# Optimization experiments

Hardware: AMD Instinct MI355X
Metric: run time of the kernel (lower is better)

The kernel has to match this reference:

```python
import jax, jax.numpy as jnp
import numpy as np

DIM = 1024
H = 16          # num query heads
KV = 8          # num kv heads
HD = DIM // H   # head_dim = 64
B, P = 8, 1024


def setup_inputs() -> dict:
    key = jax.random.key(0)
    ks = jax.random.split(key, 6)
    s = 0.02
    return {
        "x": jax.random.normal(ks[0], (B, P, DIM), dtype=jnp.float32),
        "Wq": jax.random.normal(ks[1], (DIM, DIM), dtype=jnp.float32) * s,
        "Wk": jax.random.normal(ks[2], (KV * HD, DIM), dtype=jnp.float32) * s,
        "Wv": jax.random.normal(ks[3], (KV * HD, DIM), dtype=jnp.float32) * s,
        "Wp": jax.random.normal(ks[4], (DIM, DIM), dtype=jnp.float32) * s,
        "bp": jax.random.normal(ks[5], (DIM,), dtype=jnp.float32) * s,
    }


def _q_allocations(k):
    # k: (B, KV, P, HD). k_norms: frobenius norm over (P, HD), summed over batch.
    kn = jnp.sqrt(jnp.sum(k * k, axis=(2, 3))).sum(axis=0)  # (KV,)
    kn = (kn - kn.min()) / (kn.max() - kn.min())
    alloc = jnp.round(kn / kn.sum() * H).astype(jnp.int32)   # (KV,)
    # fix up so alloc.sum() == H (mirrors the torch while-loops)
    alloc = jax.lax.while_loop(lambda a: a.sum() > H,
                               lambda a: a.at[jnp.argmax(a)].add(-1), alloc)
    alloc = jax.lax.while_loop(lambda a: a.sum() < H,
                               lambda a: a.at[jnp.argmin(a)].add(1), alloc)
    return alloc


def reference(x, Wq, Wk, Wv, Wp, bp):
    Bx, Px, C = x.shape
    scale = HD ** -0.5
    q = (x @ Wq.T).reshape(Bx, Px, H, HD).transpose(0, 2, 1, 3) * scale  # (B,H,P,HD)
    k = (x @ Wk.T).reshape(Bx, Px, KV, HD).transpose(0, 2, 1, 3)         # (B,KV,P,HD)
    v = (x @ Wv.T).reshape(Bx, Px, KV, HD).transpose(0, 2, 1, 3)

    alloc = _q_allocations(k)  # (KV,) sums to H
    # query head h belongs to kv group i where cumsum[i-1] <= h < cumsum[i].
    # Equivalent to torch.split(q, alloc) + per-group attention, because the
    # per-group softmax over keys is independent per query head.
    kv_idx = jnp.searchsorted(jnp.cumsum(alloc), jnp.arange(H), side='right')
    k_g = jnp.take(k, kv_idx, axis=1)  # (B,H,P,HD)
    v_g = jnp.take(v, kv_idx, axis=1)

    scores = jnp.einsum('bhqd,bhkd->bhqk', q, k_g)
    weights = jax.nn.softmax(scores, axis=-1)
    out = jnp.einsum('bhqk,bhkd->bhqd', weights, v_g)  # (B,H,P,HD)
    out = out.transpose(0, 2, 1, 3).reshape(Bx, Px, C)
    return out @ Wp.T + bp
```

## Files before the change

### kernel.cpp

```cpp
#include <hip/hip_runtime.h>
#include <stdint.h>


typedef float f32x4 __attribute__((ext_vector_type(4)));
typedef short s16x8 __attribute__((ext_vector_type(8)));
typedef short s16x4 __attribute__((ext_vector_type(4)));
typedef int   i32x4 __attribute__((ext_vector_type(4)));

__device__ __forceinline__ unsigned short f2bf(float f) {
  unsigned int u = __builtin_bit_cast(unsigned int, f);
  u = (u + 0x7FFFu + ((u >> 16) & 1u)) >> 16;
  return (unsigned short)u;
}
__device__ __forceinline__ float bf2f(unsigned short h) {
  unsigned int u = ((unsigned int)h) << 16;
  return __builtin_bit_cast(float, u);
}

__device__ __forceinline__ unsigned int pk_bf16(float a, float b) {
#if __has_builtin(__builtin_amdgcn_cvt_pk_bf16_f32)
  auto v = __builtin_amdgcn_cvt_pk_bf16_f32(a, b);
  return __builtin_bit_cast(unsigned int, v);
#else
  unsigned int ua = __builtin_bit_cast(unsigned int, a);
  unsigned int ub = __builtin_bit_cast(unsigned int, b);
  ua += 0x7FFFu + ((ua >> 16) & 1u);
  ub += 0x7FFFu + ((ub >> 16) & 1u);
#if __has_builtin(__builtin_amdgcn_perm)
  return __builtin_amdgcn_perm(ub, ua, 0x07060302);
#else
  return (ua >> 16) | (ub & 0xFFFF0000u);
#endif
#endif
}

__device__ __forceinline__ unsigned int perm_half(unsigned int hi, unsigned int lo, int takeHi) {
#if __has_builtin(__builtin_amdgcn_perm)
  return __builtin_amdgcn_perm(hi, lo, takeHi ? 0x07060302u : 0x05040100u);
#else
  return takeHi ? ((lo >> 16) | (hi & 0xFFFF0000u)) : ((lo & 0xFFFFu) | (hi << 16));
#endif
}

__device__ __forceinline__ float fast_exp2(float x) {
#if __has_builtin(__builtin_amdgcn_exp2f)
  return __builtin_amdgcn_exp2f(x);
#else
  return exp2f(x);
#endif
}

#if __has_builtin(__builtin_amdgcn_global_load_lds)
#define HAVE_GLL 1
typedef const __attribute__((address_space(1))) void* gas_ptr;
typedef __attribute__((address_space(3))) void* las_ptr;
__device__ __forceinline__ void gll16(const void* g, void* l) {
  __builtin_amdgcn_global_load_lds((gas_ptr)g, (las_ptr)l, 16, 0, 0);
}
#endif

__global__ void convert_kernel(const float* __restrict__ x, const float* __restrict__ Wq,
                               const float* __restrict__ Wk, const float* __restrict__ Wv,
                               const float* __restrict__ Wp,
                               unsigned short* __restrict__ xb,
                               unsigned short* __restrict__ wqkv,
                               unsigned short* __restrict__ wpb,
                               float* __restrict__ sums) {
  if (blockIdx.x == 0 && threadIdx.x < 64) sums[threadIdx.x] = 0.0f;
  const long i = ((long)blockIdx.x * 256 + threadIdx.x) * 4;
  const float* src; unsigned short* dst; long off; float scale = 1.0f;
  if (i < 8388608L)       { src = x;  dst = xb;             off = i;             }
  else if (i < 9437184L)  { src = Wq; dst = wqkv;           off = i - 8388608L;  scale = 0.18033688011112042f; }
  else if (i < 9961472L)  { src = Wk; dst = wqkv + 1048576; off = i - 9437184L;  }
  else if (i < 10485760L) { src = Wv; dst = wqkv + 1572864; off = i - 9961472L;  }
  else                    { src = Wp; dst = wpb;            off = i - 10485760L; }
  f32x4 v = *(const f32x4*)(src + off);
  s16x4 o;
  o[0] = (short)f2bf(v[0] * scale);
  o[1] = (short)f2bf(v[1] * scale);
  o[2] = (short)f2bf(v[2] * scale);
  o[3] = (short)f2bf(v[3] * scale);
  *(s16x4*)(dst + off) = o;
}

template<int N, bool OUT_BF16, bool DO_SUMSQ>
__global__ __launch_bounds__(256)
void gemm_bt(const unsigned short* __restrict__ A,
             const unsigned short* __restrict__ Bw,
             unsigned short* __restrict__ Cb,
             float* __restrict__ Cf,
             const float* __restrict__ bias,
             float* __restrict__ sums) {
  __shared__ __align__(16) unsigned short As[8192];
  __shared__ __align__(16) unsigned short Bs[8192];
  constexpr int NB = N / 128;
  const int bm = blockIdx.x / NB, bn = blockIdx.x % NB;
  const int m0 = bm * 128, n0 = bn * 128;
  const int t = threadIdx.x;
  const int w = t >> 6, lane = t & 63, quad = lane >> 4, ln = lane & 15;
  const int wm = w & 1, wn = w >> 1;

  const int lrow = lane >> 3;
  const int lc8  = ((lane & 7) ^ lrow) << 3;
  const unsigned short* agl = A  + (m0 + w * 32 + lrow) * 1024 + lc8;
  const unsigned short* bgl = Bw + (n0 + w * 32 + lrow) * 1024 + lc8;

  f32x4 acc[4][4] = {};

  for (int k0 = 0; k0 < 1024; k0 += 64) {
    __syncthreads();
#ifdef HAVE_GLL
    #pragma unroll
    for (int c = 0; c < 4; ++c) {
      gll16(agl + k0 + c * 8192, &As[w * 2048 + c * 512]);
      gll16(bgl + k0 + c * 8192, &Bs[w * 2048 + c * 512]);
    }
#else
    i32x4 ra[4], rb[4];
    #pragma unroll
    for (int c = 0; c < 4; ++c) {
      ra[c] = *(const i32x4*)(agl + k0 + c * 8192);
      rb[c] = *(const i32x4*)(bgl + k0 + c * 8192);
    }
    #pragma unroll
    for (int c = 0; c < 4; ++c) {
      *(i32x4*)(&As[w * 2048 + c * 512 + lane * 8]) = ra[c];
      *(i32x4*)(&Bs[w * 2048 + c * 512 + lane * 8]) = rb[c];
    }
#endif
    __syncthreads();
    #pragma unroll
    for (int kc = 0; kc < 2; ++kc) {
      const int pcs = ((kc * 4 + quad) ^ (ln & 7)) << 3;
      s16x8 af[4], bf[4];
      #pragma unroll
      for (int i = 0; i < 4; ++i)
        af[i] = *(const s16x8*)(&As[(wm * 64 + i * 16 + ln) * 64 + pcs]);
      #pragma unroll
      for (int j = 0; j < 4; ++j)
        bf[j] = *(const s16x8*)(&Bs[(wn * 64 + j * 16 + ln) * 64 + pcs]);
      #pragma unroll
      for (int i = 0; i < 4; ++i)
        #pragma unroll
        for (int j = 0; j < 4; ++j)
          acc[i][j] = __builtin_amdgcn_mfma_f32_16x16x32_bf16(af[i], bf[j], acc[i][j], 0, 0, 0);
    }
  }

  if constexpr (DO_SUMSQ) {
    if (bn >= 8 && bn < 12) {
      float ss = 0.0f;
      #pragma unroll
      for (int i = 0; i < 4; ++i)
        #pragma unroll
        for (int j = 0; j < 4; ++j)
          #pragma unroll
          for (int r = 0; r < 4; ++r)
            ss += acc[i][j][r] * acc[i][j][r];
      #pragma unroll
      for (int off = 1; off < 64; off <<= 1) ss += __shfl_xor(ss, off);
      if (lane == 0)
        atomicAdd(&sums[(m0 >> 10) * 8 + (bn - 8) * 2 + wn], ss);
    }
  }

  #pragma unroll
  for (int j = 0; j < 4; ++j) {
    const int gn = n0 + wn * 64 + j * 16 + ln;
    float bv = 0.0f;
    if constexpr (!OUT_BF16) bv = bias[gn];
    #pragma unroll
    for (int i = 0; i < 4; ++i) {
      const int gm0 = m0 + wm * 64 + i * 16 + quad * 4;
      #pragma unroll
      for (int r = 0; r < 4; ++r) {
        float v = acc[i][j][r];
        if constexpr (OUT_BF16) Cb[(gm0 + r) * N + gn] = f2bf(v);
        else                    Cf[(gm0 + r) * N + gn] = v + bv;
      }
    }
  }
}

__global__ __launch_bounds__(256, 4)
void attn_kernel(const unsigned short* __restrict__ qkv,
                 const float* __restrict__ sums,
                 unsigned short* __restrict__ att) {
  __shared__ __align__(16) unsigned short Ks[4096];
  __shared__ __align__(16) unsigned short Vt[64][72];
  __shared__ __align__(16) unsigned int  Plb[4][32][36];
  __shared__ int kvs;

  const int bid = blockIdx.x;
  const int h = bid & 15, qt = (bid >> 4) & 7, b = bid >> 7;
  const int t = threadIdx.x, w = t >> 6, lane = t & 63, quad = lane >> 4, ln = lane & 15;

  if (t == 0) {
    float kn[8];
    for (int kv = 0; kv < 8; ++kv) {
      float s = 0.0f;
      for (int bb = 0; bb < 8; ++bb) s += sqrtf(sums[bb * 8 + kv]);
      kn[kv] = s;
    }
    float mn = kn[0], mx = kn[0];
    for (int i = 1; i < 8; ++i) { mn = fminf(mn, kn[i]); mx = fmaxf(mx, kn[i]); }
    float tot = 0.0f;
    for (int i = 0; i < 8; ++i) { kn[i] = (kn[i] - mn) / (mx - mn); tot += kn[i]; }
    int a[8], sum = 0;
    for (int i = 0; i < 8; ++i) { a[i] = (int)rintf(kn[i] * 16.0f / tot); sum += a[i]; }
    while (sum > 16) {
      int im = 0;
      for (int i = 1; i < 8; ++i) if (a[i] > a[im]) im = i;
      a[im]--; sum--;
    }
    while (sum < 16) {
      int im = 0;
      for (int i = 1; i < 8; ++i) if (a[i] < a[im]) im = i;
      a[im]++; sum++;
    }
    int cum = 0, idx = 0, c[8];
    for (int i = 0; i < 8; ++i) { cum += a[i]; c[i] = cum; }
    while (c[idx] <= h) idx++;
    kvs = idx;
  }
  __syncthreads();
  const int kvi = kvs;

  s16x8 qf[2][2];
  #pragma unroll
  for (int s = 0; s < 2; ++s) {
    const unsigned short* qp = qkv + (b * 1024 + qt * 128 + s * 64 + w * 16 + ln) * 2048
                               + h * 64 + quad * 8;
    qf[s][0] = *(const s16x8*)(qp);
    qf[s][1] = *(const s16x8*)(qp + 32);
  }

  const int lc8 = ((lane & 7) ^ (lane >> 3)) << 3;
  const unsigned short* kglA = qkv + (b * 1024 + w * 16 + (lane >> 3)) * 2048
                               + 1024 + kvi * 64 + lc8;
  const unsigned short* kglB = kglA + 8 * 2048;

  const int kp = t & 31, vd0 = (t >> 5) << 3;
  const unsigned short* vbase = qkv + (b * 1024 + 2 * kp) * 2048 + 1536 + kvi * 64 + vd0;

  s16x8 ones;
  #pragma unroll
  for (int j = 0; j < 8; ++j) ones[j] = (short)0x3F80;

  f32x4 Oa[2][4] = {};
  f32x4 lacc[2] = {};

  s16x8 va0 = *(const s16x8*)(vbase);
  s16x8 va1 = *(const s16x8*)(vbase + 2048);

  for (int kt = 0; kt < 16; ++kt) {
    __syncthreads();
#ifdef HAVE_GLL
    gll16(kglA + kt * 131072, Ks + w * 1024);
    gll16(kglB + kt * 131072, Ks + w * 1024 + 512);
#else
    i32x4 t0 = *(const i32x4*)(kglA + kt * 131072);
    i32x4 t1 = *(const i32x4*)(kglB + kt * 131072);
    *(i32x4*)(Ks + w * 1024 + lane * 8) = t0;
    *(i32x4*)(Ks + w * 1024 + 512 + lane * 8) = t1;
#endif
    #pragma unroll
    for (int i = 0; i < 8; ++i) {
      unsigned int pk = (unsigned int)(unsigned short)va0[i] |
                        ((unsigned int)(unsigned short)va1[i] << 16);
      *(unsigned int*)(&Vt[vd0 + i][2 * kp]) = pk;
    }
    __syncthreads();

    if (kt < 15) {
      const unsigned short* q = vbase + (kt + 1) * 131072;
      va0 = *(const s16x8*)(q);
      va1 = *(const s16x8*)(q + 2048);
    }

    #pragma unroll
    for (int s = 0; s < 2; ++s) {
      f32x4 sacc[4] = {};
      #pragma unroll
      for (int ks = 0; ks < 4; ++ks) {
        const int r0 = (ks * 16 + ln) * 64;
        s16x8 kf0 = *(const s16x8*)(Ks + r0 + (((quad    ) ^ (ln & 7)) << 3));
        s16x8 kf1 = *(const s16x8*)(Ks + r0 + (((quad + 4) ^ (ln & 7)) << 3));
        sacc[ks] = __builtin_amdgcn_mfma_f32_16x16x32_bf16(qf[s][0], kf0, sacc[ks], 0, 0, 0);
        sacc[ks] = __builtin_amdgcn_mfma_f32_16x16x32_bf16(qf[s][1], kf1, sacc[ks], 0, 0, 0);
      }
      #pragma unroll
      for (int r = 0; r < 4; ++r) {
        unsigned int d0 = pk_bf16(fast_exp2(sacc[0][r]), fast_exp2(sacc[1][r]));
        unsigned int d1 = pk_bf16(fast_exp2(sacc[2][r]), fast_exp2(sacc[3][r]));
        unsigned int* pr = &Plb[w][s * 16 + quad * 4 + r][0];
        pr[ln]      = d0;
        pr[ln + 16] = d1;
      }
    }
    __asm__ volatile("s_waitcnt lgkmcnt(0)" ::: "memory");

    #pragma unroll
    for (int kc = 0; kc < 2; ++kc) {
      s16x8 pf[2];
      #pragma unroll
      for (int s = 0; s < 2; ++s) {
        const unsigned int* base = &Plb[w][s * 16 + ln][kc * 16 + (quad & 1) * 8];
        i32x4 u0 = *(const i32x4*)(base);
        i32x4 u1 = *(const i32x4*)(base + 4);
        const int th = quad >> 1;
        i32x4 pp;
        pp[0] = (int)perm_half((unsigned)u0[1], (unsigned)u0[0], th);
        pp[1] = (int)perm_half((unsigned)u0[3], (unsigned)u0[2], th);
        pp[2] = (int)perm_half((unsigned)u1[1], (unsigned)u1[0], th);
        pp[3] = (int)perm_half((unsigned)u1[3], (unsigned)u1[2], th);
        pf[s] = __builtin_bit_cast(s16x8, pp);
      }
      #pragma unroll
      for (int ds = 0; ds < 4; ++ds) {
        s16x8 vf = *(const s16x8*)(&Vt[ds * 16 + ln][kc * 32 + quad * 8]);
        Oa[0][ds] = __builtin_amdgcn_mfma_f32_16x16x32_bf16(pf[0], vf, Oa[0][ds], 0, 0, 0);
        Oa[1][ds] = __builtin_amdgcn_mfma_f32_16x16x32_bf16(pf[1], vf, Oa[1][ds], 0, 0, 0);
      }
      lacc[0] = __builtin_amdgcn_mfma_f32_16x16x32_bf16(pf[0], ones, lacc[0], 0, 0, 0);
      lacc[1] = __builtin_amdgcn_mfma_f32_16x16x32_bf16(pf[1], ones, lacc[1], 0, 0, 0);
    }
  }

  #pragma unroll
  for (int s = 0; s < 2; ++s) {
    float inv[4];
    #pragma unroll
    for (int r = 0; r < 4; ++r) inv[r] = 1.0f / lacc[s][r];
    const int orow = b * 1024 + qt * 128 + s * 64 + w * 16 + quad * 4;
    #pragma unroll
    for (int ds = 0; ds < 4; ++ds)
      #pragma unroll
      for (int r = 0; r < 4; ++r)
        att[(orow + r) * 1024 + h * 64 + ds * 16 + ln] = f2bf(Oa[s][ds][r] * inv[r]);
  }
}

extern "C" void kernel_launch(void* const* d_in, const int* in_sizes, int n_in,
                              void* d_out, int out_size, void* d_ws, size_t ws_size,
                              hipStream_t stream) {
  const float* x  = (const float*)d_in[0];
  const float* Wq = (const float*)d_in[1];
  const float* Wk = (const float*)d_in[2];
  const float* Wv = (const float*)d_in[3];
  const float* Wp = (const float*)d_in[4];
  const float* bp = (const float*)d_in[5];

  char* ws = (char*)d_ws;
  unsigned short* xb   = (unsigned short*)(ws);
  unsigned short* wqkv = (unsigned short*)(ws + 16777216);
  unsigned short* wpb  = (unsigned short*)(ws + 20971520);
  unsigned short* qkv  = (unsigned short*)(ws + 23068672);
  float*          sums = (float*)(ws + 56623104);
  unsigned short* att  = xb;

  convert_kernel<<<11264, 256, 0, stream>>>(x, Wq, Wk, Wv, Wp, xb, wqkv, wpb, sums);
  gemm_bt<2048, true, true><<<1024, 256, 0, stream>>>(xb, wqkv, qkv, nullptr, nullptr, sums);
  attn_kernel<<<1024, 256, 0, stream>>>(qkv, sums, att);
  gemm_bt<1024, false, false><<<512, 256, 0, stream>>>(att, wpb, nullptr, (float*)d_out, bp, nullptr);
}
```

Measured before the change: 219.9 us.

## Load K fragments directly from global into registers, dropping the LDS K tile

The attention kernel stops staging K tiles through shared memory. Each wave now loads its K MFMA fragments straight from global memory into registers, prefetching the next tile while the current one is processed. This removes the LDS writes, swizzled reads and some synchronization traffic for K. In exchange every wave redundantly fetches the full K tile from global/L2 and register pressure rises, so launch bounds drop from 4 to 3 blocks per CU.

```diff
diff --git a/kernel.cpp b/kernel.cpp
--- a/kernel.cpp
+++ b/kernel.cpp
@@ -11,10 +11,6 @@
   unsigned int u = __builtin_bit_cast(unsigned int, f);
   u = (u + 0x7FFFu + ((u >> 16) & 1u)) >> 16;
   return (unsigned short)u;
-}
-__device__ __forceinline__ float bf2f(unsigned short h) {
-  unsigned int u = ((unsigned int)h) << 16;
-  return __builtin_bit_cast(float, u);
 }
 
 __device__ __forceinline__ unsigned int pk_bf16(float a, float b) {
@@ -182,11 +178,10 @@
   }
 }
 
-__global__ __launch_bounds__(256, 4)
+__global__ __launch_bounds__(256, 3)
 void attn_kernel(const unsigned short* __restrict__ qkv,
                  const float* __restrict__ sums,
                  unsigned short* __restrict__ att) {
-  __shared__ __align__(16) unsigned short Ks[4096];
   __shared__ __align__(16) unsigned short Vt[64][72];
   __shared__ __align__(16) unsigned int  Plb[4][32][36];
   __shared__ int kvs;
@@ -235,10 +230,7 @@
     qf[s][1] = *(const s16x8*)(qp + 32);
   }
 
-  const int lc8 = ((lane & 7) ^ (lane >> 3)) << 3;
-  const unsigned short* kglA = qkv + (b * 1024 + w * 16 + (lane >> 3)) * 2048
-                               + 1024 + kvi * 64 + lc8;
-  const unsigned short* kglB = kglA + 8 * 2048;
+  const unsigned short* kg0 = qkv + (b * 1024 + ln) * 2048 + 1024 + kvi * 64 + quad * 8;
 
   const int kp = t & 31, vd0 = (t >> 5) << 3;
   const unsigned short* vbase = qkv + (b * 1024 + 2 * kp) * 2048 + 1536 + kvi * 64 + vd0;
@@ -252,18 +244,15 @@
 
   s16x8 va0 = *(const s16x8*)(vbase);
   s16x8 va1 = *(const s16x8*)(vbase + 2048);
+  s16x8 kf[2][4];
+  #pragma unroll
+  for (int kc = 0; kc < 2; ++kc)
+    #pragma unroll
+    for (int ks = 0; ks < 4; ++ks)
+      kf[kc][ks] = *(const s16x8*)(kg0 + (long)(ks * 16) * 2048 + kc * 32);
 
   for (int kt = 0; kt < 16; ++kt) {
     __syncthreads();
-#ifdef HAVE_GLL
-    gll16(kglA + kt * 131072, Ks + w * 1024);
-    gll16(kglB + kt * 131072, Ks + w * 1024 + 512);
-#else
-    i32x4 t0 = *(const i32x4*)(kglA + kt * 131072);
-    i32x4 t1 = *(const i32x4*)(kglB + kt * 131072);
-    *(i32x4*)(Ks + w * 1024 + lane * 8) = t0;
-    *(i32x4*)(Ks + w * 1024 + 512 + lane * 8) = t1;
-#endif
     #pragma unroll
     for (int i = 0; i < 8; ++i) {
       unsigned int pk = (unsigned int)(unsigned short)va0[i] |
@@ -283,11 +272,8 @@
       f32x4 sacc[4] = {};
       #pragma unroll
       for (int ks = 0; ks < 4; ++ks) {
-        const int r0 = (ks * 16 + ln) * 64;
-        s16x8 kf0 = *(const s16x8*)(Ks + r0 + (((quad    ) ^ (ln & 7)) << 3));
-        s16x8 kf1 = *(const s16x8*)(Ks + r0 + (((quad + 4) ^ (ln & 7)) << 3));
-        sacc[ks] = __builtin_amdgcn_mfma_f32_16x16x32_bf16(qf[s][0], kf0, sacc[ks], 0, 0, 0);
-        sacc[ks] = __builtin_amdgcn_mfma_f32_16x16x32_bf16(qf[s][1], kf1, sacc[ks], 0, 0, 0);
+        sacc[ks] = __builtin_amdgcn_mfma_f32_16x16x32_bf16(qf[s][0], kf[0][ks], sacc[ks], 0, 0, 0);
+        sacc[ks] = __builtin_amdgcn_mfma_f32_16x16x32_bf16(qf[s][1], kf[1][ks], sacc[ks], 0, 0, 0);
       }
       #pragma unroll
       for (int r = 0; r < 4; ++r) {
@@ -298,6 +284,16 @@
         pr[ln + 16] = d1;
       }
     }
+
+    if (kt < 15) {
+      const unsigned short* kgt = kg0 + (long)(kt + 1) * 131072;
+      #pragma unroll
+      for (int kc = 0; kc < 2; ++kc)
+        #pragma unroll
+        for (int ks = 0; ks < 4; ++ks)
+          kf[kc][ks] = *(const s16x8*)(kgt + (long)(ks * 16) * 2048 + kc * 32);
+    }
+
     __asm__ volatile("s_waitcnt lgkmcnt(0)" ::: "memory");
 
     #pragma unroll
```

After: 262.8 us. 19.5% more time.
